# Kernel optimization log

Hardware: AMD Instinct MI355X
Metric: run time of the kernel (lower is better)

The kernel has to match this reference:

```python
import jax, jax.numpy as jnp
import numpy as np

N, NFEAT, NHID, NCLASS, NLAYERS = 10000, 512, 256, 40, 8
LAMDA, ALPHA = 0.5, 0.1
EDGE_P = 0.003  # avg degree ~30


def setup_inputs() -> dict:
    key = jax.random.key(0)
    ks = jax.random.split(key, 8)
    x = jax.random.normal(ks[0], (N, NFEAT), dtype=jnp.float32)
    # binary adjacency with zero diagonal (normalize_adj asserts diag==0)
    adj = (jax.random.uniform(ks[1], (N, N)) < EDGE_P).astype(jnp.float32)
    adj = adj * (1.0 - jnp.eye(N, dtype=jnp.float32))
    # GraphConvolution.reset_parameters: uniform(-1/sqrt(out), 1/sqrt(out))
    s = 1.0 / np.sqrt(NHID)
    conv_w = jax.random.uniform(ks[2], (NLAYERS, NHID, NHID), jnp.float32, -s, s)
    s0 = 1.0 / np.sqrt(NFEAT)
    w0 = jax.random.uniform(ks[3], (NFEAT, NHID), jnp.float32, -s0, s0)
    b0 = jax.random.uniform(ks[4], (NHID,), jnp.float32, -s0, s0)
    s1 = 1.0 / np.sqrt(NHID)
    w1 = jax.random.uniform(ks[5], (NHID, NCLASS), jnp.float32, -s1, s1)
    b1 = jax.random.uniform(ks[6], (NCLASS,), jnp.float32, -s1, s1)
    return {"x": x, "adj": adj, "w0": w0, "b0": b0, "conv_w": conv_w, "w1": w1, "b1": b1}


def reference(x, adj, w0, b0, conv_w, w1, b1):
    n = adj.shape[0]
    # normalize_adj: A_hat = A + I; D^{-1/2} A_hat D^{-1/2}
    a_hat = adj + jnp.eye(n, dtype=adj.dtype)
    d_inv_sqrt = jax.lax.rsqrt(jnp.sum(a_hat, axis=1))
    a_norm = a_hat * d_inv_sqrt[:, None] * d_inv_sqrt[None, :]

    # dropout is a no-op in eval mode
    h0 = jax.nn.relu(x @ w0 + b0)  # [N, NHID]
    thetas = jnp.log(LAMDA / jnp.arange(1, NLAYERS + 1, dtype=jnp.float32) + 1.0)

    def step(h, wt):
        w, theta = wt
        hi = a_norm @ h                              # aggregation
        support = (1.0 - ALPHA) * hi + ALPHA * h0    # initial-residual mix (variant=False: r = support)
        out = theta * (support @ w) + (1.0 - theta) * support
        return jax.nn.relu(out), None

    h, _ = jax.lax.scan(step, h0, (conv_w, thetas))
    logits = h @ w1 + b1  # [N, NCLASS]
    return jax.nn.log_softmax(logits, axis=1)
```

## Files before the change

### kernel.cpp

```cpp
#include <hip/hip_runtime.h>
#include <math.h>

#define NN 10000
#define NFEAT 512
#define NHID 256
#define NCLASS 40
#define NLAYERS 8
#define MAXDEG 96

#define CVX_BLOCKS 5000
#define PW_BLOCKS  2560
#define PE_BLOCKS  3750

typedef __attribute__((ext_vector_type(8))) short bf16x8;
typedef __attribute__((ext_vector_type(4))) float floatx4;
typedef __attribute__((ext_vector_type(2))) float floatx2;
typedef __attribute__((ext_vector_type(4))) unsigned short ushort4v;

__device__ __forceinline__ unsigned short f2bf(float f) {
    union { float f; unsigned int u; } v; v.f = f;
    unsigned int r = v.u + 0x7fffu + ((v.u >> 16) & 1u);
    return (unsigned short)(r >> 16);
}
__device__ __forceinline__ float bf2f(unsigned short h) {
    union { unsigned int u; float f; } v; v.u = ((unsigned int)h) << 16;
    return v.f;
}
__device__ __forceinline__ unsigned char f2fp8(float f) {
    return (unsigned char)(__builtin_amdgcn_cvt_pk_fp8_f32(f, f, 0, false) & 0xFF);
}

__global__ __launch_bounds__(256) void build_graph(const float* __restrict__ adj,
                                                   int* __restrict__ cnt,
                                                   int* __restrict__ ell,
                                                   float* __restrict__ dinv) {
    int i = blockIdx.x;
    __shared__ int scnt;
    if (threadIdx.x == 0) scnt = 0;
    __syncthreads();
    const float4* row = (const float4*)(adj + (size_t)i * NN);
    const int nv = NN / 4;
    int* erow = ell + (size_t)i * MAXDEG;
    for (int f = threadIdx.x; f < nv; f += 256) {
        float4 v = row[f];
        if (v.x != 0.0f) { int s = atomicAdd(&scnt, 1); if (s < MAXDEG) erow[s] = 4*f + 0; }
        if (v.y != 0.0f) { int s = atomicAdd(&scnt, 1); if (s < MAXDEG) erow[s] = 4*f + 1; }
        if (v.z != 0.0f) { int s = atomicAdd(&scnt, 1); if (s < MAXDEG) erow[s] = 4*f + 2; }
        if (v.w != 0.0f) { int s = atomicAdd(&scnt, 1); if (s < MAXDEG) erow[s] = 4*f + 3; }
    }
    __syncthreads();
    if (threadIdx.x == 0) {
        int c = scnt;
        cnt[i] = (c < MAXDEG) ? c : MAXDEG;
        dinv[i] = rsqrtf(1.0f + (float)c);
    }
}

__global__ __launch_bounds__(256) void prep_all(const float* __restrict__ x,
                                                unsigned short* __restrict__ xb,
                                                const float* __restrict__ w0,
                                                const float* __restrict__ cw,
                                                unsigned short* __restrict__ w0t,
                                                unsigned short* __restrict__ Mt,
                                                const int* __restrict__ ell,
                                                const int* __restrict__ cnt,
                                                const float* __restrict__ dinv,
                                                int2* __restrict__ es) {
    int b = blockIdx.x, t = threadIdx.x;
    if (b < CVX_BLOCKS) {
        int idx = b * 256 + t;
        float4 v = ((const float4*)x)[idx];
        ushort4v o;
        o.x = f2bf(v.x); o.y = f2bf(v.y); o.z = f2bf(v.z); o.w = f2bf(v.w);
        ((ushort4v*)xb)[idx] = o;
    } else if (b < CVX_BLOCKS + PW_BLOCKS) {
        int idx = (b - CVX_BLOCKS) * 256 + t;
        if (idx < 131072) {
            int n = idx >> 9, k = idx & 511;
            w0t[idx] = f2bf(w0[(size_t)k * 256 + n]);
        } else {
            int j = idx - 131072;
            int l = j >> 16;
            int r = j & 65535;
            int n = r >> 8, k = r & 255;
            float theta = logf(0.5f / (float)(l + 1) + 1.0f);
            float v = theta * cw[(size_t)l * 65536 + (size_t)k * 256 + n];
            if (k == n) v += 1.0f - theta;
            Mt[j] = f2bf(v);
        }
    } else {
        int idx = (b - CVX_BLOCKS - PW_BLOCKS) * 256 + t;
        if (idx >= NN * MAXDEG) return;
        int i = idx / MAXDEG, e = idx % MAXDEG;
        int2 v; v.x = 0; v.y = 0;
        if (e < cnt[i]) {
            int j = ell[idx];
            v.x = j; v.y = __float_as_int(dinv[j]);
        }
        es[idx] = v;
    }
}

__global__ __launch_bounds__(512, 4) void gemm0_mfma(const unsigned short* __restrict__ xb,
                                                     const unsigned short* __restrict__ w0t,
                                                     const float* __restrict__ b0,
                                                     unsigned short* __restrict__ h0b,
                                                     unsigned char* __restrict__ h8o) {
    int t = threadIdx.x, wv = t >> 6, lane = t & 63;
    int lrow = lane & 15, quad = lane >> 4;
    int r0 = blockIdx.x * 16;

    bf16x8 a[16];
    const unsigned short* arow = xb + (size_t)(r0 + lrow) * NFEAT + quad * 8;
    #pragma unroll
    for (int f = 0; f < 16; ++f)
        a[f] = *(const bf16x8*)(arow + f * 32);

    #pragma unroll 1
    for (int n = 0; n < 2; ++n) {
        int nt = wv * 2 + n;
        floatx4 acc = {0.f, 0.f, 0.f, 0.f};
        const unsigned short* wrow = w0t + (size_t)(nt * 16 + lrow) * NFEAT + quad * 8;
        #pragma unroll
        for (int f = 0; f < 16; ++f) {
            bf16x8 b = *(const bf16x8*)(wrow + f * 32);
            acc = __builtin_amdgcn_mfma_f32_16x16x32_bf16(a[f], b, acc, 0, 0, 0);
        }
        int col = nt * 16 + lrow;
        float bias = b0[col];
        #pragma unroll
        for (int r = 0; r < 4; ++r) {
            int row = r0 + quad * 4 + r;
            unsigned short bv = f2bf(fmaxf(acc[r] + bias, 0.f));
            h0b[(size_t)row * NHID + col] = bv;
            h8o[(size_t)row * NHID + col] = f2fp8(bf2f(bv));
        }
    }
}

__device__ __forceinline__ void load_hg(const int2* __restrict__ e0r,
                                        const int2* __restrict__ e1r,
                                        const unsigned int* __restrict__ h8,
                                        int lane, int base,
                                        unsigned int (&x0)[4], unsigned int (&x1)[4],
                                        float (&s0)[4], float (&s1)[4]) {
    #pragma unroll
    for (int u = 0; u < 4; ++u) {
        int2 p = e0r[base + u];
        int2 q = e1r[base + u];
        s0[u] = __int_as_float(p.y);
        s1[u] = __int_as_float(q.y);
        x0[u] = h8[(size_t)p.x * 64 + lane];
        x1[u] = h8[(size_t)q.x * 64 + lane];
    }
}

__device__ __forceinline__ void proc_hg(const unsigned int (&x0)[4],
                                        const unsigned int (&x1)[4],
                                        const float (&s0)[4], const float (&s1)[4],
                                        float4& a0, float4& a1) {
    #pragma unroll
    for (int u = 0; u < 4; ++u) {
        floatx2 lo = __builtin_amdgcn_cvt_pk_f32_fp8(x0[u], false);
        floatx2 hi = __builtin_amdgcn_cvt_pk_f32_fp8(x0[u], true);
        a0.x = fmaf(s0[u], lo.x, a0.x);
        a0.y = fmaf(s0[u], lo.y, a0.y);
        a0.z = fmaf(s0[u], hi.x, a0.z);
        a0.w = fmaf(s0[u], hi.y, a0.w);
        lo = __builtin_amdgcn_cvt_pk_f32_fp8(x1[u], false);
        hi = __builtin_amdgcn_cvt_pk_f32_fp8(x1[u], true);
        a1.x = fmaf(s1[u], lo.x, a1.x);
        a1.y = fmaf(s1[u], lo.y, a1.y);
        a1.z = fmaf(s1[u], hi.x, a1.z);
        a1.w = fmaf(s1[u], hi.y, a1.w);
    }
}

template<bool LAST>
__global__ __launch_bounds__(512, 6) void layer_fused(const unsigned int* __restrict__ h8,
                                                      const unsigned short* __restrict__ h0b,
                                                      const float* __restrict__ dinv,
                                                      const int* __restrict__ cnt,
                                                      const int2* __restrict__ es,
                                                      const unsigned short* __restrict__ Mt,
                                                      const float* __restrict__ w1,
                                                      const float* __restrict__ b1,
                                                      unsigned char* __restrict__ h8_out,
                                                      float* __restrict__ out) {
    __shared__ unsigned short supb[16][264];
    __shared__ float hs[LAST ? 16 * 264 : 4];

    int t = threadIdx.x;
    int wv = __builtin_amdgcn_readfirstlane(t >> 6);
    int lane = t & 63;
    int r0 = blockIdx.x * 16;

    int lr0 = wv * 2, lr1 = lr0 + 1;
    int i0 = r0 + lr0, i1 = r0 + lr1;

    unsigned int su0 = h8[(size_t)i0 * 64 + lane];
    unsigned int su1 = h8[(size_t)i1 * 64 + lane];
    ushort4v h0v0 = ((const ushort4v*)h0b)[(size_t)i0 * 64 + lane];
    ushort4v h0v1 = ((const ushort4v*)h0b)[(size_t)i1 * 64 + lane];

    float di0 = dinv[i0], di1 = dinv[i1];
    int dA = (cnt[i0] + 7) & ~7, dB = (cnt[i1] + 7) & ~7;
    int dm = dA > dB ? dA : dB;
    const int2* e0r = es + (size_t)i0 * MAXDEG;
    const int2* e1r = es + (size_t)i1 * MAXDEG;

    floatx2 slo = __builtin_amdgcn_cvt_pk_f32_fp8(su0, false);
    floatx2 shi = __builtin_amdgcn_cvt_pk_f32_fp8(su0, true);
    float4 a0, a1;
    a0.x = di0 * slo.x; a0.y = di0 * slo.y; a0.z = di0 * shi.x; a0.w = di0 * shi.y;
    slo = __builtin_amdgcn_cvt_pk_f32_fp8(su1, false);
    shi = __builtin_amdgcn_cvt_pk_f32_fp8(su1, true);
    a1.x = di1 * slo.x; a1.y = di1 * slo.y; a1.z = di1 * shi.x; a1.w = di1 * shi.y;

    unsigned int xA0[4], xA1[4], xB0[4], xB1[4];
    float sA0[4], sA1[4], sB0[4], sB1[4];
    int nh = dm >> 2;
    if (nh > 0) {
        load_hg(e0r, e1r, h8, lane, 0, xA0, xA1, sA0, sA1);
        bool useA = true;
        #pragma unroll 1
        for (int g = 1; g < nh; ++g) {
            if (useA) {
                load_hg(e0r, e1r, h8, lane, g << 2, xB0, xB1, sB0, sB1);
                proc_hg(xA0, xA1, sA0, sA1, a0, a1);
            } else {
                load_hg(e0r, e1r, h8, lane, g << 2, xA0, xA1, sA0, sA1);
                proc_hg(xB0, xB1, sB0, sB1, a0, a1);
            }
            useA = !useA;
        }
        if (useA) proc_hg(xA0, xA1, sA0, sA1, a0, a1);
        else      proc_hg(xB0, xB1, sB0, sB1, a0, a1);
    }

    ushort4v ob;
    ob.x = f2bf(0.9f * (di0 * a0.x) + 0.1f * bf2f(h0v0.x));
    ob.y = f2bf(0.9f * (di0 * a0.y) + 0.1f * bf2f(h0v0.y));
    ob.z = f2bf(0.9f * (di0 * a0.z) + 0.1f * bf2f(h0v0.z));
    ob.w = f2bf(0.9f * (di0 * a0.w) + 0.1f * bf2f(h0v0.w));
    *(ushort4v*)&supb[lr0][4 * lane] = ob;
    ob.x = f2bf(0.9f * (di1 * a1.x) + 0.1f * bf2f(h0v1.x));
    ob.y = f2bf(0.9f * (di1 * a1.y) + 0.1f * bf2f(h0v1.y));
    ob.z = f2bf(0.9f * (di1 * a1.z) + 0.1f * bf2f(h0v1.z));
    ob.w = f2bf(0.9f * (di1 * a1.w) + 0.1f * bf2f(h0v1.w));
    *(ushort4v*)&supb[lr1][4 * lane] = ob;
    __syncthreads();

    int lrow = lane & 15, quad = lane >> 4;
    bf16x8 a[8];
    #pragma unroll
    for (int f = 0; f < 8; ++f)
        a[f] = *(const bf16x8*)&supb[lrow][quad * 8 + f * 32];

    #pragma unroll 1
    for (int n = 0; n < 2; ++n) {
        int nt = wv * 2 + n;
        floatx4 acc = {0.f, 0.f, 0.f, 0.f};
        const unsigned short* wrow = Mt + (size_t)(nt * 16 + lrow) * NHID + quad * 8;
        #pragma unroll
        for (int f = 0; f < 8; ++f) {
            bf16x8 b = *(const bf16x8*)(wrow + f * 32);
            acc = __builtin_amdgcn_mfma_f32_16x16x32_bf16(a[f], b, acc, 0, 0, 0);
        }
        int col = nt * 16 + lrow;
        #pragma unroll
        for (int r = 0; r < 4; ++r) {
            int lr2 = quad * 4 + r;
            float o = fmaxf(acc[r], 0.f);
            if (LAST) {
                hs[lr2 * 264 + col] = o;
            } else {
                h8_out[(size_t)(r0 + lr2) * NHID + col] = f2fp8(o);
            }
        }
    }

    if (LAST) {
        __syncthreads();
        #pragma unroll 1
        for (int rr = 0; rr < 2; ++rr) {
            int lr = wv * 2 + rr;
            const float* hr = hs + lr * 264;
            float logit = -1e30f;
            if (lane < NCLASS) {
                float acc = b1[lane];
                #pragma unroll 8
                for (int k = 0; k < NHID; ++k)
                    acc = fmaf(hr[k], w1[k * NCLASS + lane], acc);
                logit = acc;
            }
            float m = logit;
            #pragma unroll
            for (int off = 32; off > 0; off >>= 1)
                m = fmaxf(m, __shfl_xor(m, off, 64));
            float e = (lane < NCLASS) ? expf(logit - m) : 0.0f;
            float ssum = e;
            #pragma unroll
            for (int off = 32; off > 0; off >>= 1)
                ssum += __shfl_xor(ssum, off, 64);
            float lse = m + logf(ssum);
            if (lane < NCLASS)
                out[(size_t)(r0 + lr) * NCLASS + lane] = logit - lse;
        }
    }
}

extern "C" void kernel_launch(void* const* d_in, const int* in_sizes, int n_in,
                              void* d_out, int out_size, void* d_ws, size_t ws_size,
                              hipStream_t stream) {
    const float* x      = (const float*)d_in[0];
    const float* adj    = (const float*)d_in[1];
    const float* w0     = (const float*)d_in[2];
    const float* b0     = (const float*)d_in[3];
    const float* conv_w = (const float*)d_in[4];
    const float* w1     = (const float*)d_in[5];
    const float* b1     = (const float*)d_in[6];
    float* out = (float*)d_out;

    char* ws = (char*)d_ws;
    size_t off = 0;
    auto alloc = [&](size_t bytes) -> void* {
        void* p = ws + off;
        off = (off + bytes + 255) & ~(size_t)255;
        return p;
    };
    float*          dinv  = (float*)alloc((size_t)NN * 4);
    int*            cnt   = (int*)  alloc((size_t)NN * 4);
    int*            ell   = (int*)  alloc((size_t)NN * MAXDEG * 4);
    int2*           es    = (int2*) alloc((size_t)NN * MAXDEG * 8);
    unsigned short* xb    = (unsigned short*)alloc((size_t)NN * NFEAT * 2);
    unsigned short* w0t   = (unsigned short*)alloc((size_t)NFEAT * NHID * 2);
    unsigned short* Mt    = (unsigned short*)alloc((size_t)NLAYERS * NHID * NHID * 2);
    unsigned short* h0b   = (unsigned short*)alloc((size_t)NN * NHID * 2);
    unsigned int*   h08   = (unsigned int*)alloc((size_t)NN * NHID);
    unsigned int*   hP8   = (unsigned int*)alloc((size_t)NN * NHID);
    unsigned int*   hQ8   = (unsigned int*)alloc((size_t)NN * NHID);

    build_graph<<<NN, 256, 0, stream>>>(adj, cnt, ell, dinv);
    prep_all<<<CVX_BLOCKS + PW_BLOCKS + PE_BLOCKS, 256, 0, stream>>>(
        x, xb, w0, conv_w, w0t, Mt, ell, cnt, dinv, es);
    gemm0_mfma<<<NN / 16, 512, 0, stream>>>(xb, w0t, b0, h0b, (unsigned char*)h08);

    const unsigned int* hc8 = h08;
    for (int l = 0; l < NLAYERS; ++l) {
        unsigned int* nxt = (l & 1) ? hQ8 : hP8;
        const unsigned short* wt = Mt + (size_t)l * NHID * NHID;
        if (l == NLAYERS - 1)
            layer_fused<true><<<NN / 16, 512, 0, stream>>>(hc8, h0b, dinv, cnt, es, wt, w1, b1, nullptr, out);
        else
            layer_fused<false><<<NN / 16, 512, 0, stream>>>(hc8, h0b, dinv, cnt, es, wt, nullptr, nullptr, (unsigned char*)nxt, nullptr);
        hc8 = nxt;
    }
}
```

Measured before the change: 777.7 us.

## Fold source-side degree scaling into stored fp8 features and gather plain ELL indices

Each layer's fp8 feature output is now pre-multiplied by 16·dinv of its row, and the first-layer output is scaled the same way. The aggregation can then add gathered neighbours without a per-edge scale, and the 16x factor keeps values in fp8 range. The int2 index/scale edge array is dropped in favour of the plain int ELL indices. Padding slots point to an extra zero row, and the gather loop now processes 8 neighbours per step instead of 4. This halves edge-metadata traffic and removes FMAs, at the cost of a slightly different fp8 quantisation and one extra row per feature buffer.

```diff
diff --git a/kernel.cpp b/kernel.cpp
--- a/kernel.cpp
+++ b/kernel.cpp
@@ -7,10 +7,12 @@
 #define NCLASS 40
 #define NLAYERS 8
 #define MAXDEG 96
+#define ZROW NN
 
 #define CVX_BLOCKS 5000
 #define PW_BLOCKS  2560
 #define PE_BLOCKS  3750
+#define ZR_BLOCKS  1
 
 typedef __attribute__((ext_vector_type(8))) short bf16x8;
 typedef __attribute__((ext_vector_type(4))) float floatx4;
@@ -39,9 +41,8 @@
     if (threadIdx.x == 0) scnt = 0;
     __syncthreads();
     const float4* row = (const float4*)(adj + (size_t)i * NN);
-    const int nv = NN / 4;
     int* erow = ell + (size_t)i * MAXDEG;
-    for (int f = threadIdx.x; f < nv; f += 256) {
+    for (int f = threadIdx.x; f < NN / 4; f += 256) {
         float4 v = row[f];
         if (v.x != 0.0f) { int s = atomicAdd(&scnt, 1); if (s < MAXDEG) erow[s] = 4*f + 0; }
         if (v.y != 0.0f) { int s = atomicAdd(&scnt, 1); if (s < MAXDEG) erow[s] = 4*f + 1; }
@@ -62,10 +63,11 @@
                                                 const float* __restrict__ cw,
                                                 unsigned short* __restrict__ w0t,
                                                 unsigned short* __restrict__ Mt,
-                                                const int* __restrict__ ell,
+                                                int* __restrict__ ell,
                                                 const int* __restrict__ cnt,
-                                                const float* __restrict__ dinv,
-                                                int2* __restrict__ es) {
+                                                unsigned int* __restrict__ h08,
+                                                unsigned int* __restrict__ hP8,
+                                                unsigned int* __restrict__ hQ8) {
     int b = blockIdx.x, t = threadIdx.x;
     if (b < CVX_BLOCKS) {
         int idx = b * 256 + t;
@@ -88,22 +90,22 @@
             if (k == n) v += 1.0f - theta;
             Mt[j] = f2bf(v);
         }
-    } else {
+    } else if (b < CVX_BLOCKS + PW_BLOCKS + PE_BLOCKS) {
         int idx = (b - CVX_BLOCKS - PW_BLOCKS) * 256 + t;
         if (idx >= NN * MAXDEG) return;
         int i = idx / MAXDEG, e = idx % MAXDEG;
-        int2 v; v.x = 0; v.y = 0;
-        if (e < cnt[i]) {
-            int j = ell[idx];
-            v.x = j; v.y = __float_as_int(dinv[j]);
-        }
-        es[idx] = v;
+        if (e >= cnt[i]) ell[idx] = ZROW;
+    } else {
+        if (t < 64)        h08[(size_t)ZROW * 64 + t] = 0u;
+        else if (t < 128)  hP8[(size_t)ZROW * 64 + (t - 64)] = 0u;
+        else if (t < 192)  hQ8[(size_t)ZROW * 64 + (t - 128)] = 0u;
     }
 }
 
 __global__ __launch_bounds__(512, 4) void gemm0_mfma(const unsigned short* __restrict__ xb,
                                                      const unsigned short* __restrict__ w0t,
                                                      const float* __restrict__ b0,
+                                                     const float* __restrict__ dinv,
                                                      unsigned short* __restrict__ h0b,
                                                      unsigned char* __restrict__ h8o) {
     int t = threadIdx.x, wv = t >> 6, lane = t & 63;
@@ -123,8 +125,8 @@
         const unsigned short* wrow = w0t + (size_t)(nt * 16 + lrow) * NFEAT + quad * 8;
         #pragma unroll
         for (int f = 0; f < 16; ++f) {
-            bf16x8 b = *(const bf16x8*)(wrow + f * 32);
-            acc = __builtin_amdgcn_mfma_f32_16x16x32_bf16(a[f], b, acc, 0, 0, 0);
+            bf16x8 bb = *(const bf16x8*)(wrow + f * 32);
+            acc = __builtin_amdgcn_mfma_f32_16x16x32_bf16(a[f], bb, acc, 0, 0, 0);
         }
         int col = nt * 16 + lrow;
         float bias = b0[col];
@@ -133,46 +135,36 @@
             int row = r0 + quad * 4 + r;
             unsigned short bv = f2bf(fmaxf(acc[r] + bias, 0.f));
             h0b[(size_t)row * NHID + col] = bv;
-            h8o[(size_t)row * NHID + col] = f2fp8(bf2f(bv));
-        }
-    }
-}
-
-__device__ __forceinline__ void load_hg(const int2* __restrict__ e0r,
-                                        const int2* __restrict__ e1r,
+            h8o[(size_t)row * NHID + col] = f2fp8(bf2f(bv) * (16.0f * dinv[row]));
+        }
+    }
+}
+
+__device__ __forceinline__ void load_g8(const int* __restrict__ e0r,
+                                        const int* __restrict__ e1r,
                                         const unsigned int* __restrict__ h8,
                                         int lane, int base,
-                                        unsigned int (&x0)[4], unsigned int (&x1)[4],
-                                        float (&s0)[4], float (&s1)[4]) {
+                                        unsigned int (&x0)[8], unsigned int (&x1)[8]) {
     #pragma unroll
-    for (int u = 0; u < 4; ++u) {
-        int2 p = e0r[base + u];
-        int2 q = e1r[base + u];
-        s0[u] = __int_as_float(p.y);
-        s1[u] = __int_as_float(q.y);
-        x0[u] = h8[(size_t)p.x * 64 + lane];
-        x1[u] = h8[(size_t)q.x * 64 + lane];
-    }
-}
-
-__device__ __forceinline__ void proc_hg(const unsigned int (&x0)[4],
-                                        const unsigned int (&x1)[4],
-                                        const float (&s0)[4], const float (&s1)[4],
+    for (int u = 0; u < 8; ++u) {
+        int j0 = e0r[base + u];
+        int j1 = e1r[base + u];
+        x0[u] = h8[(size_t)j0 * 64 + lane];
+        x1[u] = h8[(size_t)j1 * 64 + lane];
+    }
+}
+
+__device__ __forceinline__ void proc_g8(const unsigned int (&x0)[8],
+                                        const unsigned int (&x1)[8],
                                         float4& a0, float4& a1) {
     #pragma unroll
-    for (int u = 0; u < 4; ++u) {
+    for (int u = 0; u < 8; ++u) {
         floatx2 lo = __builtin_amdgcn_cvt_pk_f32_fp8(x0[u], false);
         floatx2 hi = __builtin_amdgcn_cvt_pk_f32_fp8(x0[u], true);
-        a0.x = fmaf(s0[u], lo.x, a0.x);
-        a0.y = fmaf(s0[u], lo.y, a0.y);
-        a0.z = fmaf(s0[u], hi.x, a0.z);
-        a0.w = fmaf(s0[u], hi.y, a0.w);
+        a0.x += lo.x; a0.y += lo.y; a0.z += hi.x; a0.w += hi.y;
         lo = __builtin_amdgcn_cvt_pk_f32_fp8(x1[u], false);
         hi = __builtin_amdgcn_cvt_pk_f32_fp8(x1[u], true);
-        a1.x = fmaf(s1[u], lo.x, a1.x);
-        a1.y = fmaf(s1[u], lo.y, a1.y);
-        a1.z = fmaf(s1[u], hi.x, a1.z);
-        a1.w = fmaf(s1[u], hi.y, a1.w);
+        a1.x += lo.x; a1.y += lo.y; a1.z += hi.x; a1.w += hi.y;
     }
 }
 
@@ -181,7 +173,7 @@
                                                       const unsigned short* __restrict__ h0b,
                                                       const float* __restrict__ dinv,
                                                       const int* __restrict__ cnt,
-                                                      const int2* __restrict__ es,
+                                                      const int* __restrict__ ell,
                                                       const unsigned short* __restrict__ Mt,
                                                       const float* __restrict__ w1,
                                                       const float* __restrict__ b1,
@@ -189,6 +181,7 @@
                                                       float* __restrict__ out) {
     __shared__ unsigned short supb[16][264];
     __shared__ float hs[LAST ? 16 * 264 : 4];
+    __shared__ float sdi16[16];
 
     int t = threadIdx.x;
     int wv = __builtin_amdgcn_readfirstlane(t >> 6);
@@ -204,39 +197,42 @@
     ushort4v h0v1 = ((const ushort4v*)h0b)[(size_t)i1 * 64 + lane];
 
     float di0 = dinv[i0], di1 = dinv[i1];
+    if (lane == 0) { sdi16[lr0] = 16.0f * di0; sdi16[lr1] = 16.0f * di1; }
     int dA = (cnt[i0] + 7) & ~7, dB = (cnt[i1] + 7) & ~7;
     int dm = dA > dB ? dA : dB;
-    const int2* e0r = es + (size_t)i0 * MAXDEG;
-    const int2* e1r = es + (size_t)i1 * MAXDEG;
+    const int* e0r = ell + (size_t)i0 * MAXDEG;
+    const int* e1r = ell + (size_t)i1 * MAXDEG;
 
     floatx2 slo = __builtin_amdgcn_cvt_pk_f32_fp8(su0, false);
     floatx2 shi = __builtin_amdgcn_cvt_pk_f32_fp8(su0, true);
     float4 a0, a1;
-    a0.x = di0 * slo.x; a0.y = di0 * slo.y; a0.z = di0 * shi.x; a0.w = di0 * shi.y;
+    a0.x = slo.x; a0.y = slo.y; a0.z = shi.x; a0.w = shi.y;
     slo = __builtin_amdgcn_cvt_pk_f32_fp8(su1, false);
     shi = __builtin_amdgcn_cvt_pk_f32_fp8(su1, true);
-    a1.x = di1 * slo.x; a1.y = di1 * slo.y; a1.z = di1 * shi.x; a1.w = di1 * shi.y;
-
-    unsigned int xA0[4], xA1[4], xB0[4], xB1[4];
-    float sA0[4], sA1[4], sB0[4], sB1[4];
-    int nh = dm >> 2;
-    if (nh > 0) {
-        load_hg(e0r, e1r, h8, lane, 0, xA0, xA1, sA0, sA1);
+    a1.x = slo.x; a1.y = slo.y; a1.z = shi.x; a1.w = shi.y;
+
+    unsigned int xA0[8], xA1[8], xB0[8], xB1[8];
+    int ng = dm >> 3;
+    if (ng > 0) {
+        load_g8(e0r, e1r, h8, lane, 0, xA0, xA1);
         bool useA = true;
         #pragma unroll 1
-        for (int g = 1; g < nh; ++g) {
+        for (int g = 1; g < ng; ++g) {
             if (useA) {
-                load_hg(e0r, e1r, h8, lane, g << 2, xB0, xB1, sB0, sB1);
-                proc_hg(xA0, xA1, sA0, sA1, a0, a1);
+                load_g8(e0r, e1r, h8, lane, g << 3, xB0, xB1);
+                proc_g8(xA0, xA1, a0, a1);
             } else {
-                load_hg(e0r, e1r, h8, lane, g << 2, xA0, xA1, sA0, sA1);
-                proc_hg(xB0, xB1, sB0, sB1, a0, a1);
+                load_g8(e0r, e1r, h8, lane, g << 3, xA0, xA1);
+                proc_g8(xB0, xB1, a0, a1);
             }
             useA = !useA;
         }
-        if (useA) proc_hg(xA0, xA1, sA0, sA1, a0, a1);
-        else      proc_hg(xB0, xB1, sB0, sB1, a0, a1);
-    }
+        if (useA) proc_g8(xA0, xA1, a0, a1);
+        else      proc_g8(xB0, xB1, a0, a1);
+    }
+
+    a0.x *= 0.0625f; a0.y *= 0.0625f; a0.z *= 0.0625f; a0.w *= 0.0625f;
+    a1.x *= 0.0625f; a1.y *= 0.0625f; a1.z *= 0.0625f; a1.w *= 0.0625f;
 
     ushort4v ob;
     ob.x = f2bf(0.9f * (di0 * a0.x) + 0.1f * bf2f(h0v0.x));
@@ -264,8 +260,8 @@
         const unsigned short* wrow = Mt + (size_t)(nt * 16 + lrow) * NHID + quad * 8;
         #pragma unroll
         for (int f = 0; f < 8; ++f) {
-            bf16x8 b = *(const bf16x8*)(wrow + f * 32);
-            acc = __builtin_amdgcn_mfma_f32_16x16x32_bf16(a[f], b, acc, 0, 0, 0);
+            bf16x8 bb = *(const bf16x8*)(wrow + f * 32);
+            acc = __builtin_amdgcn_mfma_f32_16x16x32_bf16(a[f], bb, acc, 0, 0, 0);
         }
         int col = nt * 16 + lrow;
         #pragma unroll
@@ -275,7 +271,7 @@
             if (LAST) {
                 hs[lr2 * 264 + col] = o;
             } else {
-                h8_out[(size_t)(r0 + lr2) * NHID + col] = f2fp8(o);
+                h8_out[(size_t)(r0 + lr2) * NHID + col] = f2fp8(o * sdi16[lr2]);
             }
         }
     }
@@ -332,28 +328,27 @@
     float*          dinv  = (float*)alloc((size_t)NN * 4);
     int*            cnt   = (int*)  alloc((size_t)NN * 4);
     int*            ell   = (int*)  alloc((size_t)NN * MAXDEG * 4);
-    int2*           es    = (int2*) alloc((size_t)NN * MAXDEG * 8);
     unsigned short* xb    = (unsigned short*)alloc((size_t)NN * NFEAT * 2);
     unsigned short* w0t   = (unsigned short*)alloc((size_t)NFEAT * NHID * 2);
     unsigned short* Mt    = (unsigned short*)alloc((size_t)NLAYERS * NHID * NHID * 2);
     unsigned short* h0b   = (unsigned short*)alloc((size_t)NN * NHID * 2);
-    unsigned int*   h08   = (unsigned int*)alloc((size_t)NN * NHID);
-    unsigned int*   hP8   = (unsigned int*)alloc((size_t)NN * NHID);
-    unsigned int*   hQ8   = (unsigned int*)alloc((size_t)NN * NHID);
+    unsigned int*   h08   = (unsigned int*)alloc((size_t)(NN + 1) * NHID);
+    unsigned int*   hP8   = (unsigned int*)alloc((size_t)(NN + 1) * NHID);
+    unsigned int*   hQ8   = (unsigned int*)alloc((size_t)(NN + 1) * NHID);
 
     build_graph<<<NN, 256, 0, stream>>>(adj, cnt, ell, dinv);
-    prep_all<<<CVX_BLOCKS + PW_BLOCKS + PE_BLOCKS, 256, 0, stream>>>(
-        x, xb, w0, conv_w, w0t, Mt, ell, cnt, dinv, es);
-    gemm0_mfma<<<NN / 16, 512, 0, stream>>>(xb, w0t, b0, h0b, (unsigned char*)h08);
+    prep_all<<<CVX_BLOCKS + PW_BLOCKS + PE_BLOCKS + ZR_BLOCKS, 256, 0, stream>>>(
+        x, xb, w0, conv_w, w0t, Mt, ell, cnt, h08, hP8, hQ8);
+    gemm0_mfma<<<NN / 16, 512, 0, stream>>>(xb, w0t, b0, dinv, h0b, (unsigned char*)h08);
 
     const unsigned int* hc8 = h08;
     for (int l = 0; l < NLAYERS; ++l) {
         unsigned int* nxt = (l & 1) ? hQ8 : hP8;
         const unsigned short* wt = Mt + (size_t)l * NHID * NHID;
         if (l == NLAYERS - 1)
-            layer_fused<true><<<NN / 16, 512, 0, stream>>>(hc8, h0b, dinv, cnt, es, wt, w1, b1, nullptr, out);
+            layer_fused<true><<<NN / 16, 512, 0, stream>>>(hc8, h0b, dinv, cnt, ell, wt, w1, b1, nullptr, out);
         else
-            layer_fused<false><<<NN / 16, 512, 0, stream>>>(hc8, h0b, dinv, cnt, es, wt, nullptr, nullptr, (unsigned char*)nxt, nullptr);
+            layer_fused<false><<<NN / 16, 512, 0, stream>>>(hc8, h0b, dinv, cnt, ell, wt, nullptr, nullptr, (unsigned char*)nxt, nullptr);
         hc8 = nxt;
     }
 }
```

Result: slower. 891.0 us (+14.6%).
